# Performance work log

Hardware: AMD Instinct MI355X
Metric: run time of the kernel (lower is better)

The kernel has to match this reference:

```python
import jax, jax.numpy as jnp
import numpy as np

B, T, D = 8, 1024, 1024

def setup_inputs() -> dict:
    key = jax.random.key(0)
    ks = jax.random.split(key, 9)
    s = D ** -0.5
    return {
        "x": jax.random.normal(ks[0], (B, T, D), dtype=jnp.float32),
        "w_q": jax.random.normal(ks[1], (D, D), dtype=jnp.float32) * s,
        "b_q": jax.random.normal(ks[2], (D,), dtype=jnp.float32) * 0.02,
        "w_k": jax.random.normal(ks[3], (D, D), dtype=jnp.float32) * s,
        "b_k": jax.random.normal(ks[4], (D,), dtype=jnp.float32) * 0.02,
        "w_v": jax.random.normal(ks[5], (D, D), dtype=jnp.float32) * s,
        "b_v": jax.random.normal(ks[6], (D,), dtype=jnp.float32) * 0.02,
        "w_o": jax.random.normal(ks[7], (D, D), dtype=jnp.float32) * s,
        "b_o": jax.random.normal(ks[8], (D,), dtype=jnp.float32) * 0.02,
    }

def reference(x, w_q, b_q, w_k, b_k, w_v, b_v, w_o, b_o):
    d = x.shape[-1]
    scale = jnp.asarray(d, x.dtype) ** -0.5
    q = jnp.einsum('btd,ed->bte', x, w_q) + b_q  # nn.Linear: x @ W^T + b
    k = jnp.einsum('btd,ed->bte', x, w_k) + b_k
    v = jnp.einsum('btd,ed->bte', x, w_v) + b_v
    t = x.shape[1]
    causal = jnp.tril(jnp.ones((t, t), dtype=bool))  # (T, T)
    scores = jnp.einsum('bqd,bkd->bqk', q, k) * scale
    scores = jnp.where(causal, scores, -jnp.inf)
    attn = jax.nn.softmax(scores, axis=-1)  # max-subtraction folded in
    out = jnp.einsum('bqk,bkd->bqd', attn, v)
    return jnp.einsum('btd,ed->bte', out, w_o) + b_o
```

## Files before the change

kernel.cpp:

```cpp
#include <hip/hip_runtime.h>

typedef unsigned short u16;
typedef __attribute__((ext_vector_type(8))) short short8;
typedef __attribute__((ext_vector_type(4))) float f32x4;


__device__ __forceinline__ u16 f2bf(float f) {
  unsigned u = __builtin_bit_cast(unsigned, f);
  u += 0x7fffu + ((u >> 16) & 1u);
  return (u16)(u >> 16);
}

__device__ __forceinline__ void gload16(const void* g, void* l) {
  __builtin_amdgcn_global_load_lds(
      (const __attribute__((address_space(1))) unsigned*)g,
      (__attribute__((address_space(3))) unsigned*)l, 16, 0, 0);
}


#define PTILE(RB_C, RB_N, DOSTAGE, VM, LAST)                                  \
  {                                                                           \
    char* cA = sA0 + cur * 49152;                                             \
                                                       \
    if (DOSTAGE) {                                                            \
      const int ns = (cur + 2 >= 3) ? cur - 1 : cur + 2;                      \
      char* dA = sA0 + ns * 49152;                                            \
      _Pragma("unroll") for (int j = 0; j < 3; ++j) {                         \
        gload16(ga[j], dA + la[j]); ga[j] += 64; }                            \
    }                                                                         \
    _Pragma("unroll") for (int kk = 0; kk < 2; ++kk)                          \
      _Pragma("unroll") for (int i = 0; i < 2; ++i) {                         \
        const int rm = wr + 32 + i * 16 + l16;                                \
        a1f[kk][i] = *(const short8*)(cA + rm * 128 +                         \
            (((kk << 2) + quad) ^ (rm & 7)) * 16);                            \
      }                                                                       \
    asm volatile("s_waitcnt lgkmcnt(4)" ::: "memory");                        \
    __builtin_amdgcn_sched_barrier(0);                                        \
    __builtin_amdgcn_s_setprio(1);                                            \
    _Pragma("unroll") for (int kk = 0; kk < 2; ++kk)                          \
      _Pragma("unroll") for (int i = 0; i < 2; ++i)                           \
        _Pragma("unroll") for (int j = 0; j < 4; ++j)                         \
          acc[i][j] = __builtin_amdgcn_mfma_f32_16x16x32_bf16(                \
              a0f[kk][i], RB_C[kk][j], acc[i][j], 0, 0, 0);                   \
    __builtin_amdgcn_s_setprio(0);                                            \
                                                       \
    if (DOSTAGE) {                                                            \
      const int ns = (cur + 2 >= 3) ? cur - 1 : cur + 2;                      \
      char* dA = sA0 + ns * 49152; char* dB = dA + 32768;                     \
      gload16(ga[3], dA + la[3]); ga[3] += 64;                                \
      _Pragma("unroll") for (int j = 0; j < 2; ++j) {                         \
        gload16(gb[j], dB + lb[j]); gb[j] += 64; }                            \
    }                                                                         \
    if (!(LAST)) {                                                            \
      asm volatile("s_waitcnt vmcnt(" #VM ") lgkmcnt(0)" ::: "memory");       \
      __builtin_amdgcn_s_barrier();                                           \
      asm volatile("" ::: "memory");                                          \
      const int nc = (cur + 1 >= 3) ? 0 : cur + 1;                            \
      char* nA = sA0 + nc * 49152; char* nB = nA + 32768;                     \
      _Pragma("unroll") for (int kk = 0; kk < 2; ++kk)                        \
        _Pragma("unroll") for (int j = 0; j < 4; ++j) {                       \
          const int rn = wc + j * 16 + l16;                                   \
          RB_N[kk][j] = *(const short8*)(nB + rn * 128 +                      \
              (((kk << 2) + quad) ^ (rn & 7)) * 16);                          \
        }                                                                     \
      _Pragma("unroll") for (int kk = 0; kk < 2; ++kk)                        \
        _Pragma("unroll") for (int i = 0; i < 2; ++i) {                       \
          const int rm = wr + i * 16 + l16;                                   \
          a0f[kk][i] = *(const short8*)(nA + rm * 128 +                       \
              (((kk << 2) + quad) ^ (rm & 7)) * 16);                          \
        }                                                                     \
    } else {                                                                  \
      asm volatile("s_waitcnt lgkmcnt(0)" ::: "memory");                      \
    }                                                                         \
    __builtin_amdgcn_sched_barrier(0);                                        \
    __builtin_amdgcn_s_setprio(1);                                            \
    _Pragma("unroll") for (int kk = 0; kk < 2; ++kk)                          \
      _Pragma("unroll") for (int i = 0; i < 2; ++i)                           \
        _Pragma("unroll") for (int j = 0; j < 4; ++j)                         \
          acc[2 + i][j] = __builtin_amdgcn_mfma_f32_16x16x32_bf16(            \
              a1f[kk][i], RB_C[kk][j], acc[2 + i][j], 0, 0, 0);               \
    __builtin_amdgcn_s_setprio(0);                                            \
    cur = (cur + 1 >= 3) ? 0 : cur + 1;                                       \
  }

__device__ __forceinline__ void gemm_256x128(
    const u16* __restrict__ A, const u16* __restrict__ B,
    int m0, int n0, char* smem, f32x4 acc[4][4])
{
  const int tid  = threadIdx.x;
  const int lane = tid & 63;
  const int quad = lane >> 4;
  const int l16  = lane & 15;
  const int wave = tid >> 6;
  const int wr   = (wave >> 1) << 6;
  const int wc   = (wave & 1) << 6;

  const u16* ga[4]; int la[4];
  const u16* gb[2]; int lb[2];
#pragma unroll
  for (int j = 0; j < 4; ++j) {
    const int L = j * 512 + tid;
    const int r = L >> 3;
    const int c = (L & 7) ^ (r & 7);
    la[j] = L * 16;
    ga[j] = A + (size_t)(m0 + r) * 1024 + c * 8;
  }
#pragma unroll
  for (int j = 0; j < 2; ++j) {
    const int L = j * 512 + tid;
    const int r = L >> 3;
    const int c = (L & 7) ^ (r & 7);
    lb[j] = L * 16;
    gb[j] = B + (size_t)(n0 + r) * 1024 + c * 8;
  }
  char* const sA0 = smem;

  short8 bfr0[2][4], bfr1[2][4];
  short8 a0f[2][2], a1f[2][2];

  {
    char* dA = sA0; char* dB = sA0 + 32768;
#pragma unroll
    for (int j = 0; j < 4; ++j) { gload16(ga[j], dA + la[j]); ga[j] += 64; }
#pragma unroll
    for (int j = 0; j < 2; ++j) { gload16(gb[j], dB + lb[j]); gb[j] += 64; }
    dA = sA0 + 49152; dB = dA + 32768;
#pragma unroll
    for (int j = 0; j < 4; ++j) { gload16(ga[j], dA + la[j]); ga[j] += 64; }
#pragma unroll
    for (int j = 0; j < 2; ++j) { gload16(gb[j], dB + lb[j]); gb[j] += 64; }
  }
  asm volatile("s_waitcnt vmcnt(6)" ::: "memory");
  __builtin_amdgcn_s_barrier();
  asm volatile("" ::: "memory");
  {
    char* nA = sA0; char* nB = sA0 + 32768;
#pragma unroll
    for (int kk = 0; kk < 2; ++kk)
#pragma unroll
      for (int j = 0; j < 4; ++j) {
        const int rn = wc + j * 16 + l16;
        bfr0[kk][j] = *(const short8*)(nB + rn * 128 + (((kk << 2) + quad) ^ (rn & 7)) * 16);
      }
#pragma unroll
    for (int kk = 0; kk < 2; ++kk)
#pragma unroll
      for (int i = 0; i < 2; ++i) {
        const int rm = wr + i * 16 + l16;
        a0f[kk][i] = *(const short8*)(nA + rm * 128 + (((kk << 2) + quad) ^ (rm & 7)) * 16);
      }
  }

  int cur = 0;
#pragma unroll 1
  for (int it = 0; it < 7; ++it) {
    PTILE(bfr0, bfr1, true, 6, false);
    PTILE(bfr1, bfr0, true, 6, false);
  }
  PTILE(bfr0, bfr1, false, 0, false);
  PTILE(bfr1, bfr0, false, 0, true);
  __syncthreads();
}

#define ACC_ZERO4(acc) { _Pragma("unroll") for (int i=0;i<4;++i) \
  _Pragma("unroll") for (int j=0;j<4;++j) \
  _Pragma("unroll") for (int r=0;r<4;++r) acc[i][j][r]=0.f; }
#define ACC_ZERO2(acc) { _Pragma("unroll") for (int i=0;i<2;++i) \
  _Pragma("unroll") for (int j=0;j<4;++j) \
  _Pragma("unroll") for (int r=0;r<4;++r) acc[i][j][r]=0.f; }

__device__ __forceinline__ void store256x128_bf16(
    f32x4 acc[4][4], const float* bias, int n0,
    u16* C, int m0, char* smem)
{
  const int tid = threadIdx.x, lane = tid & 63, wave = tid >> 6;
  const int quad = lane >> 4, l16 = lane & 15;
  const int wr = (wave >> 1) << 6, wc = (wave & 1) << 6;
  u16* t = (u16*)smem;
#pragma unroll
  for (int j = 0; j < 4; ++j) {
    const int nn = wc + j * 16 + l16;
    const float bj = bias[n0 + nn];
#pragma unroll
    for (int i = 0; i < 4; ++i) {
      const int mm = wr + i * 16 + quad * 4;
#pragma unroll
      for (int r = 0; r < 4; ++r)
        t[(mm + r) * 136 + nn] = f2bf(acc[i][j][r] + bj);
    }
  }
  __syncthreads();
#pragma unroll
  for (int it = 0; it < 8; ++it) {
    const int L = it * 512 + tid;
    const int mm = L >> 4, cc = L & 15;
    *(uint4*)(C + (size_t)(m0 + mm) * 1024 + n0 + cc * 8) =
        *(const uint4*)(t + mm * 136 + cc * 8);
  }
}

__device__ __forceinline__ void gemm_tile_64(
    const u16* __restrict__ A, int lda,
    const u16* __restrict__ B, int ldb,
    int m0, int n0, int kend,
    char* sA, char* sB, f32x4 acc[2][4])
{
  const int tid  = threadIdx.x;
  const int lane = tid & 63;
  const int wave = tid >> 6;
  const int quad = lane >> 4;
  const int l16  = lane & 15;
  const int wr   = (wave >> 1) << 5;
  const int wc   = (wave & 1) << 6;

  const u16* ga[2]; int la[2];
  const u16* gb[4]; int lb[4];
#pragma unroll
  for (int j = 0; j < 2; ++j) {
    const int Lb = j * 256 + wave * 64;
    const int L  = Lb + lane;
    const int r  = L >> 3;
    const int c  = (L & 7) ^ (r & 7);
    la[j] = Lb * 16;
    ga[j] = A + (size_t)(m0 + r) * lda + c * 8;
  }
#pragma unroll
  for (int j = 0; j < 4; ++j) {
    const int Lb = j * 256 + wave * 64;
    const int L  = Lb + lane;
    const int r  = L >> 3;
    const int c  = (L & 7) ^ (r & 7);
    lb[j] = Lb * 16;
    gb[j] = B + (size_t)(n0 + r) * ldb + c * 8;
  }

  for (int kt = 0; kt < kend; kt += 64) {
#pragma unroll
    for (int j = 0; j < 2; ++j) { gload16(ga[j], sA + la[j]); ga[j] += 64; }
#pragma unroll
    for (int j = 0; j < 4; ++j) { gload16(gb[j], sB + lb[j]); gb[j] += 64; }
    __syncthreads();
#pragma unroll
    for (int kk = 0; kk < 2; ++kk) {
      short8 af[2], bfr[4];
#pragma unroll
      for (int i = 0; i < 2; ++i) {
        const int rm = wr + i * 16 + l16;
        af[i] = *(const short8*)(sA + rm * 128 + (((kk << 2) + quad) ^ (rm & 7)) * 16);
      }
#pragma unroll
      for (int j = 0; j < 4; ++j) {
        const int rn = wc + j * 16 + l16;
        bfr[j] = *(const short8*)(sB + rn * 128 + (((kk << 2) + quad) ^ (rn & 7)) * 16);
      }
#pragma unroll
      for (int i = 0; i < 2; ++i)
#pragma unroll
        for (int j = 0; j < 4; ++j)
          acc[i][j] = __builtin_amdgcn_mfma_f32_16x16x32_bf16(af[i], bfr[j], acc[i][j], 0, 0, 0);
    }
    __syncthreads();
  }
}

__global__ __launch_bounds__(256) void cast_inputs(
    const float* __restrict__ x,  const float* __restrict__ wq,
    const float* __restrict__ wk, const float* __restrict__ wv,
    const float* __restrict__ wo,
    u16* xb, u16* wqb, u16* wkb, u16* wvb, u16* wob, float* rsum)
{
  int b = blockIdx.x;
  if (b < 8) {
    float4 z = {0.f, 0.f, 0.f, 0.f};
    *(float4*)(rsum + (b * 256 + threadIdx.x) * 4) = z;
  }
  const float* src; u16* dst; int base;
  if (b < 4096) { src = x; dst = xb; base = b * 2048; }
  else {
    int r = (b - 4096) >> 9, bb = (b - 4096) & 511;
    base = bb * 2048;
    src = (r == 0) ? wq : (r == 1) ? wk : (r == 2) ? wv : wo;
    dst = (r == 0) ? wqb : (r == 1) ? wkb : (r == 2) ? wvb : wob;
  }
  int i0 = base + threadIdx.x * 8;
  float4 f0 = *(const float4*)(src + i0);
  float4 f1 = *(const float4*)(src + i0 + 4);
  short8 o;
  o[0]=(short)f2bf(f0.x); o[1]=(short)f2bf(f0.y); o[2]=(short)f2bf(f0.z); o[3]=(short)f2bf(f0.w);
  o[4]=(short)f2bf(f1.x); o[5]=(short)f2bf(f1.y); o[6]=(short)f2bf(f1.z); o[7]=(short)f2bf(f1.w);
  *(short8*)(dst + i0) = o;
}

__global__ __launch_bounds__(512, 2) void proj_qkv(
    const u16* __restrict__ xb,
    const u16* __restrict__ wqb, const u16* __restrict__ wkb, const u16* __restrict__ wvb,
    const float* __restrict__ bq, const float* __restrict__ bk, const float* __restrict__ bv,
    u16* q, u16* k, u16* vt)
{
  __shared__ char smem[147456];
  const int z = blockIdx.y;
  const u16* W = (z == 0) ? wqb : (z == 1) ? wkb : wvb;
  const float* bias = (z == 0) ? bq : (z == 1) ? bk : bv;
  const int id = blockIdx.x;
  const int m0 = ((id & 7) * 4 + ((id >> 3) & 3)) * 256;
  const int n0 = (id >> 5) * 128;

  f32x4 acc[4][4]; ACC_ZERO4(acc);
  gemm_256x128(xb, W, m0, n0, smem, acc);

  if (z < 2) {
    store256x128_bf16(acc, bias, n0, (z == 0) ? q : k, m0, smem);
  } else {
    const int tid = threadIdx.x, lane = tid & 63, wave = tid >> 6;
    const int quad = lane >> 4, l16 = lane & 15;
    const int wr = (wave >> 1) << 6, wc = (wave & 1) << 6;
    u16* t = (u16*)smem;
#pragma unroll
    for (int j = 0; j < 4; ++j) {
      const int nn = wc + j * 16 + l16;
      const float bj = bias[n0 + nn];
#pragma unroll
      for (int i = 0; i < 4; ++i) {
        const int mm = wr + i * 16 + quad * 4;
#pragma unroll
        for (int r = 0; r < 4; ++r)
          t[nn * 264 + mm + r] = f2bf(acc[i][j][r] + bj);
      }
    }
    __syncthreads();
    const int b = m0 >> 10, t0 = m0 & 1023;
#pragma unroll
    for (int it = 0; it < 8; ++it) {
      const int L = it * 512 + tid;
      const int nn = L >> 5, cc = L & 31;
      *(uint4*)(vt + ((size_t)b << 20) + (size_t)(n0 + nn) * 1024 + t0 + cc * 8) =
          *(const uint4*)(t + nn * 264 + cc * 8);
    }
  }
}

__global__ __launch_bounds__(256) void qk_expscores(
    const u16* __restrict__ q, const u16* __restrict__ k,
    u16* __restrict__ probs, float* __restrict__ rowsum)
{
  const int id = blockIdx.x;
  const int b = id / 72, t = id - b * 72;
  int p = (int)((__builtin_sqrtf((float)(4 * t + 1)) - 1.f) * 0.5f);
  while ((p + 1) * (p + 2) <= t) ++p;
  while (p * (p + 1) > t) --p;
  int r0 = t - p * (p + 1);
  const int qi = 2 * p + (r0 >= p + 1);
  const int kb = (r0 >= p + 1) ? r0 - (p + 1) : r0;

  __shared__ char smem[24576];
  char* sA = smem; char* sB = smem + 8192;
  const u16* A = q + ((size_t)b << 20);
  const u16* B = k + ((size_t)b << 20);
  const int m0 = qi * 64, n0 = kb * 128;

  f32x4 acc[2][4]; ACC_ZERO2(acc);
  gemm_tile_64(A, 1024, B, 1024, m0, n0, 1024, sA, sB, acc);

  const int tid = threadIdx.x, lane = tid & 63, wave = tid >> 6;
  const int quad = lane >> 4, l16 = lane & 15;
  const int wr = (wave >> 1) << 5, wc = (wave & 1) << 6;
  const bool diag = (kb == (qi >> 1));

  float part[2][4];
#pragma unroll
  for (int i = 0; i < 2; ++i)
#pragma unroll
    for (int r = 0; r < 4; ++r) part[i][r] = 0.f;

  u16* tl = (u16*)smem;
#pragma unroll
  for (int j = 0; j < 4; ++j) {
    const int nn = wc + j * 16 + l16;
#pragma unroll
    for (int i = 0; i < 2; ++i) {
      const int mm = wr + i * 16 + quad * 4;
#pragma unroll
      for (int r = 0; r < 4; ++r) {
        float e = __expf(acc[i][j][r] * 0.03125f);
        if (diag && (n0 + nn) > (m0 + mm + r)) e = 0.f;
        part[i][r] += e;
        tl[(mm + r) * 136 + nn] = f2bf(e);
      }
    }
  }
  float* rs = rowsum + b * 1024 + m0;
#pragma unroll
  for (int i = 0; i < 2; ++i)
#pragma unroll
    for (int r = 0; r < 4; ++r) {
      float v = part[i][r];
      v += __shfl_xor(v, 1); v += __shfl_xor(v, 2);
      v += __shfl_xor(v, 4); v += __shfl_xor(v, 8);
      if (l16 == 0) atomicAdd(rs + wr + i * 16 + quad * 4 + r, v);
    }
  __syncthreads();
  u16* C = probs + ((size_t)b << 20);
#pragma unroll
  for (int it = 0; it < 4; ++it) {
    const int L = it * 256 + tid;
    const int mm = L >> 4, cc = L & 15;
    *(uint4*)(C + (size_t)(m0 + mm) * 1024 + n0 + cc * 8) =
        *(const uint4*)(tl + mm * 136 + cc * 8);
  }
}

__global__ __launch_bounds__(256) void pv_gemm(
    const u16* __restrict__ probs, const u16* __restrict__ vt,
    const float* __restrict__ rowsum, u16* __restrict__ o)
{
  const int id = blockIdx.x;
  const int b = id & 7, nb = (id >> 3) & 7, qi = 15 - (id >> 6);
  __shared__ char smem[24576];
  char* sA = smem; char* sB = smem + 8192;
  const u16* A = probs + ((size_t)b << 20);
  const u16* B = vt + ((size_t)b << 20);
  const int m0 = qi * 64, n0 = nb * 128;
  const int kend = (qi + 1) * 64;

  f32x4 acc[2][4]; ACC_ZERO2(acc);
  gemm_tile_64(A, 1024, B, 1024, m0, n0, kend, sA, sB, acc);

  const int tid = threadIdx.x, lane = tid & 63, wave = tid >> 6;
  const int quad = lane >> 4, l16 = lane & 15;
  const int wr = (wave >> 1) << 5, wc = (wave & 1) << 6;
  const float* rs = rowsum + b * 1024 + m0;
  u16* tl = (u16*)smem;
#pragma unroll
  for (int i = 0; i < 2; ++i)
#pragma unroll
    for (int r = 0; r < 4; ++r) {
      const int mm = wr + i * 16 + quad * 4 + r;
      const float inv = 1.0f / rs[mm];
#pragma unroll
      for (int j = 0; j < 4; ++j)
        tl[mm * 136 + wc + j * 16 + l16] = f2bf(acc[i][j][r] * inv);
    }
  __syncthreads();
  u16* C = o + ((size_t)b << 20);
#pragma unroll
  for (int it = 0; it < 4; ++it) {
    const int L = it * 256 + tid;
    const int mm = L >> 4, cc = L & 15;
    *(uint4*)(C + (size_t)(m0 + mm) * 1024 + n0 + cc * 8) =
        *(const uint4*)(tl + mm * 136 + cc * 8);
  }
}

__global__ __launch_bounds__(512, 2) void proj_o(
    const u16* __restrict__ ob, const u16* __restrict__ wob,
    const float* __restrict__ bo, float* __restrict__ out)
{
  __shared__ char smem[147456];
  const int id = blockIdx.x;
  const int m0 = ((id & 7) * 4 + ((id >> 3) & 3)) * 256;
  const int n0 = (id >> 5) * 128;
  f32x4 acc[4][4]; ACC_ZERO4(acc);
  gemm_256x128(ob, wob, m0, n0, smem, acc);

  const int tid = threadIdx.x, lane = tid & 63, wave = tid >> 6;
  const int quad = lane >> 4, l16 = lane & 15;
  const int wr = (wave >> 1) << 6, wc = (wave & 1) << 6;
  float* tf = (float*)smem;
#pragma unroll
  for (int j = 0; j < 4; ++j) {
    const int nn = wc + j * 16 + l16;
    const float bj = bo[n0 + nn];
#pragma unroll
    for (int i = 0; i < 4; ++i)
#pragma unroll
      for (int r = 0; r < 4; ++r)
        tf[(wr + i * 16 + quad * 4 + r) * 132 + nn] = acc[i][j][r] + bj;
  }
  __syncthreads();
#pragma unroll
  for (int it = 0; it < 16; ++it) {
    const int L = it * 512 + tid;
    const int mm = L >> 5, cc = L & 31;
    *(float4*)(out + (size_t)(m0 + mm) * 1024 + n0 + cc * 4) =
        *(const float4*)(tf + mm * 132 + cc * 4);
  }
}

extern "C" void kernel_launch(void* const* d_in, const int* in_sizes, int n_in,
                              void* d_out, int out_size, void* d_ws, size_t ws_size,
                              hipStream_t stream) {
  const float* x  = (const float*)d_in[0];
  const float* wq = (const float*)d_in[1];
  const float* bq = (const float*)d_in[2];
  const float* wk = (const float*)d_in[3];
  const float* bk = (const float*)d_in[4];
  const float* wv = (const float*)d_in[5];
  const float* bv = (const float*)d_in[6];
  const float* wo = (const float*)d_in[7];
  const float* bo = (const float*)d_in[8];
  float* out = (float*)d_out;

  char* ws = (char*)d_ws;
  const size_t MB = 1u << 20;
  u16*  xb  = (u16*)(ws);
  u16*  wqb = (u16*)(ws + 16*MB);
  u16*  wkb = (u16*)(ws + 18*MB);
  u16*  wvb = (u16*)(ws + 20*MB);
  u16*  wob = (u16*)(ws + 22*MB);
  u16*  qb  = (u16*)(ws + 24*MB);
  u16*  kb  = (u16*)(ws + 40*MB);
  u16*  vtb = (u16*)(ws + 56*MB);
  u16*  pr  = (u16*)(ws + 72*MB);
  float* rsum = (float*)(ws + 88*MB);

  cast_inputs<<<6144, 256, 0, stream>>>(x, wq, wk, wv, wo, xb, wqb, wkb, wvb, wob, rsum);
  proj_qkv<<<dim3(256, 3), 512, 0, stream>>>(xb, wqb, wkb, wvb, bq, bk, bv, qb, kb, vtb);
  qk_expscores<<<576, 256, 0, stream>>>(qb, kb, pr, rsum);
  pv_gemm<<<1024, 256, 0, stream>>>(pr, vtb, rsum, xb );
  proj_o<<<256, 512, 0, stream>>>(xb, wob, bo, out);
}
```

Baseline: 225.9 us.

## Reuse pipelined 256x128 GEMM tile for causal QK^T and PV kernels

Drops the simple 64x128 single-buffered attention GEMM tile. The QK^T-exp and PV kernels now call the triple-buffered 256x128 GEMM used by the projections, which takes a new tile-count argument so PV can stop at the causal boundary. The aim is more operand reuse per block and better overlap of global loads with MFMA work. In exchange the grids become much coarser (160 and 256 blocks of 512 threads), which risks load imbalance and idle CUs. Coarser causal tiles also waste some work on masked regions, and the causal mask is now checked on every tile.

```diff
diff --git a/kernel.cpp b/kernel.cpp
--- a/kernel.cpp
+++ b/kernel.cpp
@@ -85,7 +85,7 @@
 
 __device__ __forceinline__ void gemm_256x128(
     const u16* __restrict__ A, const u16* __restrict__ B,
-    int m0, int n0, char* smem, f32x4 acc[4][4])
+    int m0, int n0, int ntiles, char* smem, f32x4 acc[4][4])
 {
   const int tid  = threadIdx.x;
   const int lane = tid & 63;
@@ -152,8 +152,9 @@
   }
 
   int cur = 0;
+  const int npair = (ntiles >> 1) - 1;
 #pragma unroll 1
-  for (int it = 0; it < 7; ++it) {
+  for (int it = 0; it < npair; ++it) {
     PTILE(bfr0, bfr1, true, 6, false);
     PTILE(bfr1, bfr0, true, 6, false);
   }
@@ -163,9 +164,6 @@
 }
 
 #define ACC_ZERO4(acc) { _Pragma("unroll") for (int i=0;i<4;++i) \
-  _Pragma("unroll") for (int j=0;j<4;++j) \
-  _Pragma("unroll") for (int r=0;r<4;++r) acc[i][j][r]=0.f; }
-#define ACC_ZERO2(acc) { _Pragma("unroll") for (int i=0;i<2;++i) \
   _Pragma("unroll") for (int j=0;j<4;++j) \
   _Pragma("unroll") for (int r=0;r<4;++r) acc[i][j][r]=0.f; }
 
@@ -196,70 +194,6 @@
     const int mm = L >> 4, cc = L & 15;
     *(uint4*)(C + (size_t)(m0 + mm) * 1024 + n0 + cc * 8) =
         *(const uint4*)(t + mm * 136 + cc * 8);
-  }
-}
-
-__device__ __forceinline__ void gemm_tile_64(
-    const u16* __restrict__ A, int lda,
-    const u16* __restrict__ B, int ldb,
-    int m0, int n0, int kend,
-    char* sA, char* sB, f32x4 acc[2][4])
-{
-  const int tid  = threadIdx.x;
-  const int lane = tid & 63;
-  const int wave = tid >> 6;
-  const int quad = lane >> 4;
-  const int l16  = lane & 15;
-  const int wr   = (wave >> 1) << 5;
-  const int wc   = (wave & 1) << 6;
-
-  const u16* ga[2]; int la[2];
-  const u16* gb[4]; int lb[4];
-#pragma unroll
-  for (int j = 0; j < 2; ++j) {
-    const int Lb = j * 256 + wave * 64;
-    const int L  = Lb + lane;
-    const int r  = L >> 3;
-    const int c  = (L & 7) ^ (r & 7);
-    la[j] = Lb * 16;
-    ga[j] = A + (size_t)(m0 + r) * lda + c * 8;
-  }
-#pragma unroll
-  for (int j = 0; j < 4; ++j) {
-    const int Lb = j * 256 + wave * 64;
-    const int L  = Lb + lane;
-    const int r  = L >> 3;
-    const int c  = (L & 7) ^ (r & 7);
-    lb[j] = Lb * 16;
-    gb[j] = B + (size_t)(n0 + r) * ldb + c * 8;
-  }
-
-  for (int kt = 0; kt < kend; kt += 64) {
-#pragma unroll
-    for (int j = 0; j < 2; ++j) { gload16(ga[j], sA + la[j]); ga[j] += 64; }
-#pragma unroll
-    for (int j = 0; j < 4; ++j) { gload16(gb[j], sB + lb[j]); gb[j] += 64; }
-    __syncthreads();
-#pragma unroll
-    for (int kk = 0; kk < 2; ++kk) {
-      short8 af[2], bfr[4];
-#pragma unroll
-      for (int i = 0; i < 2; ++i) {
-        const int rm = wr + i * 16 + l16;
-        af[i] = *(const short8*)(sA + rm * 128 + (((kk << 2) + quad) ^ (rm & 7)) * 16);
-      }
-#pragma unroll
-      for (int j = 0; j < 4; ++j) {
-        const int rn = wc + j * 16 + l16;
-        bfr[j] = *(const short8*)(sB + rn * 128 + (((kk << 2) + quad) ^ (rn & 7)) * 16);
-      }
-#pragma unroll
-      for (int i = 0; i < 2; ++i)
-#pragma unroll
-        for (int j = 0; j < 4; ++j)
-          acc[i][j] = __builtin_amdgcn_mfma_f32_16x16x32_bf16(af[i], bfr[j], acc[i][j], 0, 0, 0);
-    }
-    __syncthreads();
   }
 }
 
@@ -306,7 +240,7 @@
   const int n0 = (id >> 5) * 128;
 
   f32x4 acc[4][4]; ACC_ZERO4(acc);
-  gemm_256x128(xb, W, m0, n0, smem, acc);
+  gemm_256x128(xb, W, m0, n0, 16, smem, acc);
 
   if (z < 2) {
     store256x128_bf16(acc, bias, n0, (z == 0) ? q : k, m0, smem);
@@ -339,36 +273,31 @@
   }
 }
 
-__global__ __launch_bounds__(256) void qk_expscores(
+__global__ __launch_bounds__(512, 2) void qk_exp256(
     const u16* __restrict__ q, const u16* __restrict__ k,
     u16* __restrict__ probs, float* __restrict__ rowsum)
 {
+  __shared__ char smem[147456];
   const int id = blockIdx.x;
-  const int b = id / 72, t = id - b * 72;
-  int p = (int)((__builtin_sqrtf((float)(4 * t + 1)) - 1.f) * 0.5f);
-  while ((p + 1) * (p + 2) <= t) ++p;
-  while (p * (p + 1) > t) --p;
-  int r0 = t - p * (p + 1);
-  const int qi = 2 * p + (r0 >= p + 1);
-  const int kb = (r0 >= p + 1) ? r0 - (p + 1) : r0;
-
-  __shared__ char smem[24576];
-  char* sA = smem; char* sB = smem + 8192;
+  const int b = id / 20;
+  const int t = id - b * 20;
+  const int qi = (t < 2) ? 0 : (t < 6) ? 1 : (t < 12) ? 2 : 3;
+  const int pre = (qi == 0) ? 0 : (qi == 1) ? 2 : (qi == 2) ? 6 : 12;
+  const int kt = t - pre;
+  const int m0 = qi * 256, n0 = kt * 128;
   const u16* A = q + ((size_t)b << 20);
   const u16* B = k + ((size_t)b << 20);
-  const int m0 = qi * 64, n0 = kb * 128;
-
-  f32x4 acc[2][4]; ACC_ZERO2(acc);
-  gemm_tile_64(A, 1024, B, 1024, m0, n0, 1024, sA, sB, acc);
+
+  f32x4 acc[4][4]; ACC_ZERO4(acc);
+  gemm_256x128(A, B, m0, n0, 16, smem, acc);
 
   const int tid = threadIdx.x, lane = tid & 63, wave = tid >> 6;
   const int quad = lane >> 4, l16 = lane & 15;
-  const int wr = (wave >> 1) << 5, wc = (wave & 1) << 6;
-  const bool diag = (kb == (qi >> 1));
-
-  float part[2][4];
-#pragma unroll
-  for (int i = 0; i < 2; ++i)
+  const int wr = (wave >> 1) << 6, wc = (wave & 1) << 6;
+
+  float part[4][4];
+#pragma unroll
+  for (int i = 0; i < 4; ++i)
 #pragma unroll
     for (int r = 0; r < 4; ++r) part[i][r] = 0.f;
 
@@ -377,12 +306,12 @@
   for (int j = 0; j < 4; ++j) {
     const int nn = wc + j * 16 + l16;
 #pragma unroll
-    for (int i = 0; i < 2; ++i) {
+    for (int i = 0; i < 4; ++i) {
       const int mm = wr + i * 16 + quad * 4;
 #pragma unroll
       for (int r = 0; r < 4; ++r) {
         float e = __expf(acc[i][j][r] * 0.03125f);
-        if (diag && (n0 + nn) > (m0 + mm + r)) e = 0.f;
+        if ((n0 + nn) > (m0 + mm + r)) e = 0.f;
         part[i][r] += e;
         tl[(mm + r) * 136 + nn] = f2bf(e);
       }
@@ -390,7 +319,7 @@
   }
   float* rs = rowsum + b * 1024 + m0;
 #pragma unroll
-  for (int i = 0; i < 2; ++i)
+  for (int i = 0; i < 4; ++i)
 #pragma unroll
     for (int r = 0; r < 4; ++r) {
       float v = part[i][r];
@@ -401,37 +330,39 @@
   __syncthreads();
   u16* C = probs + ((size_t)b << 20);
 #pragma unroll
-  for (int it = 0; it < 4; ++it) {
-    const int L = it * 256 + tid;
+  for (int it = 0; it < 8; ++it) {
+    const int L = it * 512 + tid;
     const int mm = L >> 4, cc = L & 15;
     *(uint4*)(C + (size_t)(m0 + mm) * 1024 + n0 + cc * 8) =
         *(const uint4*)(tl + mm * 136 + cc * 8);
   }
 }
 
-__global__ __launch_bounds__(256) void pv_gemm(
+__global__ __launch_bounds__(512, 2) void pv256(
     const u16* __restrict__ probs, const u16* __restrict__ vt,
     const float* __restrict__ rowsum, u16* __restrict__ o)
 {
+  __shared__ char smem[147456];
   const int id = blockIdx.x;
-  const int b = id & 7, nb = (id >> 3) & 7, qi = 15 - (id >> 6);
-  __shared__ char smem[24576];
-  char* sA = smem; char* sB = smem + 8192;
+  const int b = id & 7;
+  const int u = id >> 3;
+  const int qi = 3 - (u & 3);
+  const int nb = u >> 2;
+  const int m0 = qi * 256, n0 = nb * 128;
+  const int nt = (qi + 1) * 4;
   const u16* A = probs + ((size_t)b << 20);
   const u16* B = vt + ((size_t)b << 20);
-  const int m0 = qi * 64, n0 = nb * 128;
-  const int kend = (qi + 1) * 64;
-
-  f32x4 acc[2][4]; ACC_ZERO2(acc);
-  gemm_tile_64(A, 1024, B, 1024, m0, n0, kend, sA, sB, acc);
+
+  f32x4 acc[4][4]; ACC_ZERO4(acc);
+  gemm_256x128(A, B, m0, n0, nt, smem, acc);
 
   const int tid = threadIdx.x, lane = tid & 63, wave = tid >> 6;
   const int quad = lane >> 4, l16 = lane & 15;
-  const int wr = (wave >> 1) << 5, wc = (wave & 1) << 6;
+  const int wr = (wave >> 1) << 6, wc = (wave & 1) << 6;
   const float* rs = rowsum + b * 1024 + m0;
   u16* tl = (u16*)smem;
 #pragma unroll
-  for (int i = 0; i < 2; ++i)
+  for (int i = 0; i < 4; ++i)
 #pragma unroll
     for (int r = 0; r < 4; ++r) {
       const int mm = wr + i * 16 + quad * 4 + r;
@@ -443,8 +374,8 @@
   __syncthreads();
   u16* C = o + ((size_t)b << 20);
 #pragma unroll
-  for (int it = 0; it < 4; ++it) {
-    const int L = it * 256 + tid;
+  for (int it = 0; it < 8; ++it) {
+    const int L = it * 512 + tid;
     const int mm = L >> 4, cc = L & 15;
     *(uint4*)(C + (size_t)(m0 + mm) * 1024 + n0 + cc * 8) =
         *(const uint4*)(tl + mm * 136 + cc * 8);
@@ -460,7 +391,7 @@
   const int m0 = ((id & 7) * 4 + ((id >> 3) & 3)) * 256;
   const int n0 = (id >> 5) * 128;
   f32x4 acc[4][4]; ACC_ZERO4(acc);
-  gemm_256x128(ob, wob, m0, n0, smem, acc);
+  gemm_256x128(ob, wob, m0, n0, 16, smem, acc);
 
   const int tid = threadIdx.x, lane = tid & 63, wave = tid >> 6;
   const int quad = lane >> 4, l16 = lane & 15;
@@ -515,7 +446,7 @@
 
   cast_inputs<<<6144, 256, 0, stream>>>(x, wq, wk, wv, wo, xb, wqb, wkb, wvb, wob, rsum);
   proj_qkv<<<dim3(256, 3), 512, 0, stream>>>(xb, wqb, wkb, wvb, bq, bk, bv, qb, kb, vtb);
-  qk_expscores<<<576, 256, 0, stream>>>(qb, kb, pr, rsum);
-  pv_gemm<<<1024, 256, 0, stream>>>(pr, vtb, rsum, xb );
+  qk_exp256<<<160, 512, 0, stream>>>(qb, kb, pr, rsum);
+  pv256<<<256, 512, 0, stream>>>(pr, vtb, rsum, xb );
   proj_o<<<256, 512, 0, stream>>>(xb, wob, bo, out);
 }
```

Result: faster. 211.9 us (-6.2%).
